# Optimization experiments

Hardware: AMD Instinct MI355X
Metric: run time of the kernel (lower is better)

The kernel has to match this reference:

```python
import jax, jax.numpy as jnp
import numpy as np

B, S, D, H, L, F = 4, 2048, 512, 8, 4, 2048
DH = D // H
EPS = 1e-5


def setup_inputs() -> dict:
    key = jax.random.key(0)
    ks = jax.random.split(key, 16)
    sc = 0.02
    inp = {
        "turn_embeddings": jax.random.normal(ks[0], (B, S, D), jnp.float32),
        "Wqkv": jax.random.normal(ks[1], (L, 3 * D, D), jnp.float32) * sc,
        "bqkv": jnp.zeros((L, 3 * D), jnp.float32),
        "Wo": jax.random.normal(ks[2], (L, D, D), jnp.float32) * sc,
        "bo": jnp.zeros((L, D), jnp.float32),
        "W1": jax.random.normal(ks[3], (L, F, D), jnp.float32) * sc,
        "b1": jnp.zeros((L, F), jnp.float32),
        "W2": jax.random.normal(ks[4], (L, D, F), jnp.float32) * sc,
        "b2": jnp.zeros((L, D), jnp.float32),
        "ln1_g": jnp.ones((L, D), jnp.float32),
        "ln1_b": jnp.zeros((L, D), jnp.float32),
        "ln2_g": jnp.ones((L, D), jnp.float32),
        "ln2_b": jnp.zeros((L, D), jnp.float32),
        "speaker_ids": jax.random.randint(ks[5], (B, S), 0, 4, jnp.int64 if jax.config.jax_enable_x64 else jnp.int32),
    }
    return inp


def _layer_norm(x, g, b):
    mu = jnp.mean(x, axis=-1, keepdims=True)
    var = jnp.mean(jnp.square(x - mu), axis=-1, keepdims=True)
    return (x - mu) * jax.lax.rsqrt(var + EPS) * g + b


def _attention(x, Wqkv, bqkv, Wo, bo, allow):
    # x: [B,S,D]; allow: [B,1,S,S] boolean (causal & same-speaker)
    qkv = x @ Wqkv.T + bqkv                       # [B,S,3D]
    q, k, v = jnp.split(qkv, 3, axis=-1)
    q = q.reshape(x.shape[0], x.shape[1], H, DH)
    k = k.reshape(x.shape[0], x.shape[1], H, DH)
    v = v.reshape(x.shape[0], x.shape[1], H, DH)
    scores = jnp.einsum("bqhd,bkhd->bhqk", q, k) / np.sqrt(DH)
    scores = jnp.where(allow, scores, jnp.finfo(scores.dtype).min)
    p = jax.nn.softmax(scores, axis=-1)
    o = jnp.einsum("bhqk,bkhd->bqhd", p, v).reshape(x.shape[0], x.shape[1], D)
    return o @ Wo.T + bo


def reference(turn_embeddings, Wqkv, bqkv, Wo, bo, W1, b1, W2, b2,
              ln1_g, ln1_b, ln2_g, ln2_b, speaker_ids):
    Bc, Sc, _ = turn_embeddings.shape
    causal = jnp.tril(jnp.ones((Sc, Sc), bool))                 # [S,S]
    same = speaker_ids[:, :, None] == speaker_ids[:, None, :]    # [B,S,S]
    allow = (same & causal)[:, None, :, :]                       # [B,1,S,S]
    x = turn_embeddings
    for l in range(L):
        a = _attention(x, Wqkv[l], bqkv[l], Wo[l], bo[l], allow)
        x = _layer_norm(x + a, ln1_g[l], ln1_b[l])
        h = jax.nn.relu(x @ W1[l].T + b1[l]) @ W2[l].T + b2[l]
        x = _layer_norm(x + h, ln2_g[l], ln2_b[l])
    return x
```

## Files before the change

### kernel.cpp

```cpp
#include <hip/hip_runtime.h>
#include <stdint.h>

#define BN 4
#define SN 2048
#define DN 512
#define HN 8
#define LN 4
#define FN 2048
#define MN (BN * SN)
#define TD (3 * DN)

typedef __attribute__((ext_vector_type(8))) __bf16 bf16x8;
typedef __attribute__((ext_vector_type(4))) float f32x4;
typedef __attribute__((ext_vector_type(8))) unsigned short ushortx8;

static __device__ __forceinline__ unsigned short f2bf(float f) {
    return __builtin_bit_cast(unsigned short, (__bf16)f);
}
static __device__ __forceinline__ float bf2f(unsigned short h) {
    return __builtin_bit_cast(float, (uint32_t)h << 16);
}

static __device__ __forceinline__ void gload16(const void* g, void* l) {
    __builtin_amdgcn_global_load_lds(
        (const __attribute__((address_space(1))) void*)g,
        (__attribute__((address_space(3))) void*)l, 16, 0, 0);
}

__global__ __launch_bounds__(256) void k_cvt_all(const float* __restrict__ Wqkv,
                                                 const float* __restrict__ Wo,
                                                 const float* __restrict__ W1,
                                                 const float* __restrict__ W2,
                                                 const float* __restrict__ te,
                                                 unsigned short* __restrict__ wqkv_b,
                                                 unsigned short* __restrict__ wo_b,
                                                 unsigned short* __restrict__ w1_b,
                                                 unsigned short* __restrict__ w2_b,
                                                 unsigned short* __restrict__ xb) {
    constexpr int G0 = LN * TD * DN / 4;
    constexpr int G1 = G0 + LN * DN * DN / 4;
    constexpr int G2 = G1 + LN * FN * DN / 4;
    constexpr int G3 = G2 + LN * DN * FN / 4;
    constexpr int G4 = G3 + MN * DN / 4;
    int i = blockIdx.x * blockDim.x + threadIdx.x;
    int stride = gridDim.x * blockDim.x;
    for (; i < G4; i += stride) {
        const float* s; unsigned short* d; int j;
        if (i < G0)      { s = Wqkv; d = wqkv_b; j = i; }
        else if (i < G1) { s = Wo;   d = wo_b;   j = i - G0; }
        else if (i < G2) { s = W1;   d = w1_b;   j = i - G1; }
        else if (i < G3) { s = W2;   d = w2_b;   j = i - G2; }
        else             { s = te;   d = xb;     j = i - G3; }
        float4 v = ((const float4*)s)[j];
        ushort4 o;
        o.x = f2bf(v.x); o.y = f2bf(v.y); o.z = f2bf(v.z); o.w = f2bf(v.w);
        ((ushort4*)d)[j] = o;
    }
}

template <int MODE, int BNT>
__global__ __launch_bounds__(256) void k_gemm(const unsigned short* __restrict__ A,
                                              const unsigned short* __restrict__ B,
                                              const float* __restrict__ bias,
                                              unsigned short* __restrict__ Cb,
                                              int M, int N, int K, int GX) {
    __shared__ __align__(16) unsigned short As[128][64];
    __shared__ __align__(16) unsigned short Bs[BNT][64];
    constexpr int NFR = BNT / 32;

    const int t = threadIdx.x;
    const int lane = t & 63;
    const int wid = t >> 6;
    const int wm = wid >> 1, wn = wid & 1;
    const int lr = lane & 15;
    const int lg = lane >> 4;

    const int nwg = gridDim.x;
    const int bid = blockIdx.x;
    const int swz = (bid & 7) * (nwg >> 3) + (bid >> 3);
    const int bx = swz % GX;
    const int by = swz / GX;

    const size_t rowA = (size_t)by * 128;
    const size_t rowB = (size_t)bx * BNT;
    const unsigned short* Ab = A + rowA * K;
    const unsigned short* Bb = B + rowB * K;

    const int srow = lane >> 3;
    const int sgran = (lane & 7) ^ srow;

    f32x4 acc[4][NFR] = {};

    for (int k0 = 0; k0 < K; k0 += 64) {
        __syncthreads();
#pragma unroll
        for (int j = 0; j < 4; ++j) {
            const int c = wid * 4 + j;
            const size_t goff = (size_t)(8 * c + srow) * K + k0 + sgran * 8;
            gload16(Ab + goff, &As[8 * c][0]);
        }
#pragma unroll
        for (int j = 0; j < NFR; ++j) {
            const int c = wid * NFR + j;
            const size_t goff = (size_t)(8 * c + srow) * K + k0 + sgran * 8;
            gload16(Bb + goff, &Bs[8 * c][0]);
        }
        __syncthreads();

#pragma unroll
        for (int h = 0; h < 2; ++h) {
            const int gp = (h * 4 + lg) ^ (lr & 7);
            bf16x8 af[4], bfr[NFR];
#pragma unroll
            for (int mi = 0; mi < 4; ++mi)
                af[mi] = *(const bf16x8*)&As[wm * 64 + mi * 16 + lr][gp * 8];
#pragma unroll
            for (int ni = 0; ni < NFR; ++ni)
                bfr[ni] = *(const bf16x8*)&Bs[wn * (BNT / 2) + ni * 16 + lr][gp * 8];
#pragma unroll
            for (int mi = 0; mi < 4; ++mi)
#pragma unroll
                for (int ni = 0; ni < NFR; ++ni)
                    acc[mi][ni] = __builtin_amdgcn_mfma_f32_16x16x32_bf16(
                        af[mi], bfr[ni], acc[mi][ni], 0, 0, 0);
        }
    }

    float bv[NFR];
#pragma unroll
    for (int ni = 0; ni < NFR; ++ni)
        bv[ni] = bias[(int)rowB + wn * (BNT / 2) + ni * 16 + lr];

#pragma unroll
    for (int mi = 0; mi < 4; ++mi) {
#pragma unroll
        for (int ni = 0; ni < NFR; ++ni) {
            int col = (int)rowB + wn * (BNT / 2) + ni * 16 + lr;
            int row0 = (int)rowA + wm * 64 + mi * 16 + lg * 4;
#pragma unroll
            for (int r = 0; r < 4; ++r) {
                float v = acc[mi][ni][r] + bv[ni];
                if (MODE == 2) v = fmaxf(v, 0.f);
                Cb[(size_t)(row0 + r) * N + col] = f2bf(v);
            }
        }
    }
}

__global__ __launch_bounds__(256) void k_attn(const unsigned short* __restrict__ qkv,
                                              const int* __restrict__ spk,
                                              unsigned short* __restrict__ o) {
    __shared__ __align__(16) unsigned short Ks[2][64][64];
    __shared__ __align__(16) unsigned short Vt[2][64][64];
    __shared__ __align__(16) unsigned short Ps[4][16][64];

    const int t = threadIdx.x;
    const int lane = t & 63;
    const int w = t >> 6;
    const int lr = lane & 15;
    const int lg = lane >> 4;
    const int l7 = lr & 7;

    const int wg = blockIdx.x;
    const int inner = wg >> 3;
    const int bh = 4 * (wg & 7) + (inner & 3);
    const int qtile = (SN / 64 - 1) - (inner >> 2);
    const int b = bh >> 3;
    const int h = bh & 7;
    const int qb = qtile * 64;

    const size_t base = (size_t)b * SN * TD;
    const unsigned short* kg = qkv + base + DN + h * 64;
    const unsigned short* vg = qkv + base + 2 * DN + h * 64;

    const float SCL = 0.125f * 1.4426950408889634f;
    const unsigned short* qptr = qkv + base + (size_t)(qb + w * 16 + lr) * TD + h * 64;
    bf16x8 aq0 = *(const bf16x8*)(qptr + lg * 8);
    bf16x8 aq1 = *(const bf16x8*)(qptr + 32 + lg * 8);
#pragma unroll
    for (int j = 0; j < 8; ++j) {
        aq0[j] = (__bf16)((float)aq0[j] * SCL);
        aq1[j] = (__bf16)((float)aq1[j] * SCL);
    }

    int sqr[4], qrow[4];
#pragma unroll
    for (int r = 0; r < 4; ++r) {
        qrow[r] = qb + w * 16 + lg * 4 + r;
        sqr[r] = spk[b * SN + qrow[r]];
    }

    const int krl = lane >> 3;
    const int kgran = (lane & 7) ^ krl;
    const int vrow = lane;
    const int vd0 = w * 16;

#pragma unroll
    for (int j = 0; j < 2; ++j)
        gload16(kg + (size_t)(w * 16 + j * 8 + krl) * TD + kgran * 8,
                &Ks[0][w * 16 + j * 8][0]);
    ushortx8 vra = *(const ushortx8*)&vg[(size_t)vrow * TD + vd0];
    ushortx8 vrb = *(const ushortx8*)&vg[(size_t)vrow * TD + vd0 + 8];
#pragma unroll
    for (int j = 0; j < 8; ++j) {
        const int vc0 = (((vrow >> 3) ^ j) << 3) + (vrow & 7);
        Vt[0][vd0 + j][vc0] = vra[j];
        Vt[0][vd0 + 8 + j][vc0] = vrb[j];
    }

    float lsum[4] = {0.f, 0.f, 0.f, 0.f};
    f32x4 acc_o[4] = {};

    const int ntiles = qtile + 1;
    for (int it = 0; it < ntiles; ++it) {
        const int k0 = it * 64;
        const int cur = it & 1;
        __syncthreads();

        const bool nx = (it + 1 < ntiles);
        if (nx) {
            const int kn = k0 + 64;
#pragma unroll
            for (int j = 0; j < 2; ++j)
                gload16(kg + (size_t)(kn + w * 16 + j * 8 + krl) * TD + kgran * 8,
                        &Ks[cur ^ 1][w * 16 + j * 8][0]);
            vra = *(const ushortx8*)&vg[(size_t)(kn + vrow) * TD + vd0];
            vrb = *(const ushortx8*)&vg[(size_t)(kn + vrow) * TD + vd0 + 8];
        }
        int skr[4];
#pragma unroll
        for (int ni = 0; ni < 4; ++ni) skr[ni] = spk[b * SN + k0 + 16 * ni + lr];

        f32x4 sc4[4] = {};
        __builtin_amdgcn_s_setprio(1);
#pragma unroll
        for (int ni = 0; ni < 4; ++ni) {
            bf16x8 bk0 = *(const bf16x8*)&Ks[cur][16 * ni + lr][(lg ^ l7) * 8];
            bf16x8 bk1 = *(const bf16x8*)&Ks[cur][16 * ni + lr][((lg + 4) ^ l7) * 8];
            sc4[ni] = __builtin_amdgcn_mfma_f32_16x16x32_bf16(aq0, bk0, sc4[ni], 0, 0, 0);
            sc4[ni] = __builtin_amdgcn_mfma_f32_16x16x32_bf16(aq1, bk1, sc4[ni], 0, 0, 0);
        }
        __builtin_amdgcn_s_setprio(0);

        const bool diag = (it == ntiles - 1);
#pragma unroll
        for (int ni = 0; ni < 4; ++ni) {
#pragma unroll
            for (int r = 0; r < 4; ++r) {
                bool allow = (skr[ni] == sqr[r]);
                if (diag) allow = allow && (16 * ni + lr <= w * 16 + lg * 4 + r);
                float p = allow ? __builtin_amdgcn_exp2f(sc4[ni][r]) : 0.f;
                lsum[r] += p;
                const int q7 = (lg * 4 + r) & 7;
                const int pg = ((2 * ni + (lr >> 3)) ^ q7) * 8 + l7;
                Ps[w][lg * 4 + r][pg] = f2bf(p);
            }
        }

        bf16x8 ap0 = *(const bf16x8*)&Ps[w][lr][(lg ^ l7) * 8];
        bf16x8 ap1 = *(const bf16x8*)&Ps[w][lr][((lg + 4) ^ l7) * 8];
        __builtin_amdgcn_s_setprio(1);
#pragma unroll
        for (int ni = 0; ni < 4; ++ni) {
            bf16x8 bv0 = *(const bf16x8*)&Vt[cur][16 * ni + lr][(lg ^ l7) * 8];
            bf16x8 bv1 = *(const bf16x8*)&Vt[cur][16 * ni + lr][((lg + 4) ^ l7) * 8];
            acc_o[ni] = __builtin_amdgcn_mfma_f32_16x16x32_bf16(ap0, bv0, acc_o[ni], 0, 0, 0);
            acc_o[ni] = __builtin_amdgcn_mfma_f32_16x16x32_bf16(ap1, bv1, acc_o[ni], 0, 0, 0);
        }
        __builtin_amdgcn_s_setprio(0);

        if (nx) {
            const int nb = cur ^ 1;
#pragma unroll
            for (int j = 0; j < 8; ++j) {
                const int vc0 = (((vrow >> 3) ^ j) << 3) + (vrow & 7);
                Vt[nb][vd0 + j][vc0] = vra[j];
                Vt[nb][vd0 + 8 + j][vc0] = vrb[j];
            }
        }
    }

#pragma unroll
    for (int r = 0; r < 4; ++r) {
        float s = lsum[r];
        s += __shfl_xor(s, 1);
        s += __shfl_xor(s, 2);
        s += __shfl_xor(s, 4);
        s += __shfl_xor(s, 8);
        float inv = 1.f / s;
#pragma unroll
        for (int ni = 0; ni < 4; ++ni) {
            int d = 16 * ni + lr;
            o[(size_t)(b * SN + qrow[r]) * DN + h * 64 + d] = f2bf(acc_o[ni][r] * inv);
        }
    }
}

template <bool XF32>
__global__ __launch_bounds__(256) void k_add_ln(const void* __restrict__ xin_,
                                                const unsigned short* __restrict__ dl,
                                                const float* __restrict__ g,
                                                const float* __restrict__ bta,
                                                unsigned short* __restrict__ xb,
                                                float* __restrict__ fout) {
    const int row = blockIdx.x * 4 + (threadIdx.x >> 6);
    const int lane = threadIdx.x & 63;
    const size_t off = (size_t)row * DN + lane * 8;
    const int c0 = lane * 8;

    float v[8];
    if (XF32) {
        const float* xin = (const float*)xin_;
        float4 a0 = *(const float4*)&xin[off];
        float4 a1 = *(const float4*)&xin[off + 4];
        v[0] = a0.x; v[1] = a0.y; v[2] = a0.z; v[3] = a0.w;
        v[4] = a1.x; v[5] = a1.y; v[6] = a1.z; v[7] = a1.w;
    } else {
        ushortx8 xa = *(const ushortx8*)&((const unsigned short*)xin_)[off];
#pragma unroll
        for (int i = 0; i < 8; ++i) v[i] = bf2f(xa[i]);
    }
    ushortx8 dd = *(const ushortx8*)&dl[off];
#pragma unroll
    for (int i = 0; i < 8; ++i) v[i] += bf2f(dd[i]);

    float s1 = 0.f, s2 = 0.f;
#pragma unroll
    for (int i = 0; i < 8; ++i) { s1 += v[i]; s2 += v[i] * v[i]; }
#pragma unroll
    for (int msk = 32; msk; msk >>= 1) {
        s1 += __shfl_xor(s1, msk);
        s2 += __shfl_xor(s2, msk);
    }
    const float mean = s1 * (1.f / 512.f);
    const float var = s2 * (1.f / 512.f) - mean * mean;
    const float rs = rsqrtf(var + 1e-5f);

    float4 g0 = *(const float4*)&g[c0];
    float4 g1 = *(const float4*)&g[c0 + 4];
    float4 b0 = *(const float4*)&bta[c0];
    float4 b1 = *(const float4*)&bta[c0 + 4];
    float gg[8] = {g0.x, g0.y, g0.z, g0.w, g1.x, g1.y, g1.z, g1.w};
    float bb[8] = {b0.x, b0.y, b0.z, b0.w, b1.x, b1.y, b1.z, b1.w};

    float y[8];
    ushortx8 ub;
#pragma unroll
    for (int i = 0; i < 8; ++i) {
        y[i] = (v[i] - mean) * rs * gg[i] + bb[i];
        ub[i] = f2bf(y[i]);
    }
    *(ushortx8*)&xb[off] = ub;
    if (fout) {
        *(float4*)&fout[off] = make_float4(y[0], y[1], y[2], y[3]);
        *(float4*)&fout[off + 4] = make_float4(y[4], y[5], y[6], y[7]);
    }
}

extern "C" void kernel_launch(void* const* d_in, const int* in_sizes, int n_in,
                              void* d_out, int out_size, void* d_ws, size_t ws_size,
                              hipStream_t stream) {
    const float* te   = (const float*)d_in[0];
    const float* Wqkv = (const float*)d_in[1];
    const float* bqkv = (const float*)d_in[2];
    const float* Wo   = (const float*)d_in[3];
    const float* bo   = (const float*)d_in[4];
    const float* W1   = (const float*)d_in[5];
    const float* b1   = (const float*)d_in[6];
    const float* W2   = (const float*)d_in[7];
    const float* b2   = (const float*)d_in[8];
    const float* g1   = (const float*)d_in[9];
    const float* be1  = (const float*)d_in[10];
    const float* g2   = (const float*)d_in[11];
    const float* be2  = (const float*)d_in[12];
    const int*   spk  = (const int*)d_in[13];
    float* out = (float*)d_out;

    char* ws = (char*)d_ws;
    size_t off = 0;
    auto alloc = [&](size_t bytes) -> char* {
        char* p = ws + off;
        off += (bytes + 255) & ~(size_t)255;
        return p;
    };
    unsigned short* wqkv_b = (unsigned short*)alloc((size_t)LN * TD * DN * 2);
    unsigned short* wo_b   = (unsigned short*)alloc((size_t)LN * DN * DN * 2);
    unsigned short* w1_b   = (unsigned short*)alloc((size_t)LN * FN * DN * 2);
    unsigned short* w2_b   = (unsigned short*)alloc((size_t)LN * DN * FN * 2);
    unsigned short* xb     = (unsigned short*)alloc((size_t)MN * DN * 2);
    unsigned short* u      = (unsigned short*)alloc((size_t)MN * FN * 2);
    unsigned short* ob     = (unsigned short*)alloc((size_t)MN * DN * 2);
    unsigned short* projb  = (unsigned short*)alloc((size_t)MN * DN * 2);
    unsigned short* qkvb = u;
    unsigned short* hb   = u;

    k_cvt_all<<<2048, 256, 0, stream>>>(Wqkv, Wo, W1, W2, te,
                                        wqkv_b, wo_b, w1_b, w2_b, xb);

    for (int l = 0; l < LN; ++l) {
        k_gemm<1, 128><<<(MN / 128) * (TD / 128), 256, 0, stream>>>(
            xb, wqkv_b + (size_t)l * TD * DN, bqkv + l * TD, qkvb,
            MN, TD, DN, TD / 128);
        k_attn<<<(SN / 64) * BN * HN, 256, 0, stream>>>(qkvb, spk, ob);
        k_gemm<1, 64><<<(MN / 128) * (DN / 64), 256, 0, stream>>>(
            ob, wo_b + (size_t)l * DN * DN, bo + l * DN, projb,
            MN, DN, DN, DN / 64);
        if (l == 0)
            k_add_ln<true><<<MN / 4, 256, 0, stream>>>(
                te, projb, g1 + l * DN, be1 + l * DN, xb, nullptr);
        else
            k_add_ln<false><<<MN / 4, 256, 0, stream>>>(
                xb, projb, g1 + l * DN, be1 + l * DN, xb, nullptr);
        k_gemm<2, 128><<<(MN / 128) * (FN / 128), 256, 0, stream>>>(
            xb, w1_b + (size_t)l * FN * DN, b1 + l * FN, hb,
            MN, FN, DN, FN / 128);
        k_gemm<1, 64><<<(MN / 128) * (DN / 64), 256, 0, stream>>>(
            hb, w2_b + (size_t)l * DN * FN, b2 + l * DN, projb,
            MN, DN, FN, DN / 64);
        k_add_ln<false><<<MN / 4, 256, 0, stream>>>(
            xb, projb, g2 + l * DN, be2 + l * DN, xb,
            (l == LN - 1) ? out : nullptr);
    }
    (void)in_sizes; (void)n_in; (void)out_size; (void)ws_size;
}
```

Before: 606.6 us.

## Transpose QK^T MFMA so each lane owns one query row in attention

Swaps the MFMA operand order so the score tile comes out transposed: each lane holds four consecutive keys for a single query row. The speaker-id check, causal mask and row-sum then work on one query per lane, so the per-row cross-lane reduction becomes two shuffles and P is written to LDS as packed 8-byte stores instead of scalar 2-byte ones. K tiles are now loaded through registers and written to LDS after the PV step, replacing the direct global-to-LDS loads. The register round-trip costs extra VGPRs and LDS write instructions in exchange for fewer LDS stores and shuffles.

```diff
diff --git a/kernel.cpp b/kernel.cpp
--- a/kernel.cpp
+++ b/kernel.cpp
@@ -172,9 +172,11 @@
     const size_t base = (size_t)b * SN * TD;
     const unsigned short* kg = qkv + base + DN + h * 64;
     const unsigned short* vg = qkv + base + 2 * DN + h * 64;
+    const int* spb = spk + b * SN;
 
     const float SCL = 0.125f * 1.4426950408889634f;
-    const unsigned short* qptr = qkv + base + (size_t)(qb + w * 16 + lr) * TD + h * 64;
+    const int qrow_t = qb + w * 16 + lr;
+    const unsigned short* qptr = qkv + base + (size_t)qrow_t * TD + h * 64;
     bf16x8 aq0 = *(const bf16x8*)(qptr + lg * 8);
     bf16x8 aq1 = *(const bf16x8*)(qptr + 32 + lg * 8);
 #pragma unroll
@@ -182,25 +184,19 @@
         aq0[j] = (__bf16)((float)aq0[j] * SCL);
         aq1[j] = (__bf16)((float)aq1[j] * SCL);
     }
-
-    int sqr[4], qrow[4];
-#pragma unroll
-    for (int r = 0; r < 4; ++r) {
-        qrow[r] = qb + w * 16 + lg * 4 + r;
-        sqr[r] = spk[b * SN + qrow[r]];
-    }
-
-    const int krl = lane >> 3;
-    const int kgran = (lane & 7) ^ krl;
+    const int sq = spb[qrow_t];
+
+    const int kr0 = t >> 3;
+    const int kgr = ((t & 7) ^ (kr0 & 7)) * 8;
     const int vrow = lane;
     const int vd0 = w * 16;
 
-#pragma unroll
-    for (int j = 0; j < 2; ++j)
-        gload16(kg + (size_t)(w * 16 + j * 8 + krl) * TD + kgran * 8,
-                &Ks[0][w * 16 + j * 8][0]);
+    uint4 kra = *(const uint4*)&kg[(size_t)kr0 * TD + (t & 7) * 8];
+    uint4 krb = *(const uint4*)&kg[(size_t)(kr0 + 32) * TD + (t & 7) * 8];
     ushortx8 vra = *(const ushortx8*)&vg[(size_t)vrow * TD + vd0];
     ushortx8 vrb = *(const ushortx8*)&vg[(size_t)vrow * TD + vd0 + 8];
+    *(uint4*)&Ks[0][kr0][kgr] = kra;
+    *(uint4*)&Ks[0][kr0 + 32][kgr] = krb;
 #pragma unroll
     for (int j = 0; j < 8; ++j) {
         const int vc0 = (((vrow >> 3) ^ j) << 3) + (vrow & 7);
@@ -208,7 +204,7 @@
         Vt[0][vd0 + 8 + j][vc0] = vrb[j];
     }
 
-    float lsum[4] = {0.f, 0.f, 0.f, 0.f};
+    float lsum = 0.f;
     f32x4 acc_o[4] = {};
 
     const int ntiles = qtile + 1;
@@ -220,41 +216,45 @@
         const bool nx = (it + 1 < ntiles);
         if (nx) {
             const int kn = k0 + 64;
-#pragma unroll
-            for (int j = 0; j < 2; ++j)
-                gload16(kg + (size_t)(kn + w * 16 + j * 8 + krl) * TD + kgran * 8,
-                        &Ks[cur ^ 1][w * 16 + j * 8][0]);
+            kra = *(const uint4*)&kg[(size_t)(kn + kr0) * TD + (t & 7) * 8];
+            krb = *(const uint4*)&kg[(size_t)(kn + kr0 + 32) * TD + (t & 7) * 8];
             vra = *(const ushortx8*)&vg[(size_t)(kn + vrow) * TD + vd0];
             vrb = *(const ushortx8*)&vg[(size_t)(kn + vrow) * TD + vd0 + 8];
         }
-        int skr[4];
-#pragma unroll
-        for (int ni = 0; ni < 4; ++ni) skr[ni] = spk[b * SN + k0 + 16 * ni + lr];
+        int4 kk[4];
+#pragma unroll
+        for (int ni = 0; ni < 4; ++ni)
+            kk[ni] = *(const int4*)&spb[k0 + 16 * ni + lg * 4];
 
         f32x4 sc4[4] = {};
         __builtin_amdgcn_s_setprio(1);
 #pragma unroll
         for (int ni = 0; ni < 4; ++ni) {
-            bf16x8 bk0 = *(const bf16x8*)&Ks[cur][16 * ni + lr][(lg ^ l7) * 8];
-            bf16x8 bk1 = *(const bf16x8*)&Ks[cur][16 * ni + lr][((lg + 4) ^ l7) * 8];
-            sc4[ni] = __builtin_amdgcn_mfma_f32_16x16x32_bf16(aq0, bk0, sc4[ni], 0, 0, 0);
-            sc4[ni] = __builtin_amdgcn_mfma_f32_16x16x32_bf16(aq1, bk1, sc4[ni], 0, 0, 0);
+            bf16x8 ak0 = *(const bf16x8*)&Ks[cur][16 * ni + lr][(lg ^ l7) * 8];
+            bf16x8 ak1 = *(const bf16x8*)&Ks[cur][16 * ni + lr][((lg + 4) ^ l7) * 8];
+            sc4[ni] = __builtin_amdgcn_mfma_f32_16x16x32_bf16(ak0, aq0, sc4[ni], 0, 0, 0);
+            sc4[ni] = __builtin_amdgcn_mfma_f32_16x16x32_bf16(ak1, aq1, sc4[ni], 0, 0, 0);
         }
         __builtin_amdgcn_s_setprio(0);
 
         const bool diag = (it == ntiles - 1);
 #pragma unroll
         for (int ni = 0; ni < 4; ++ni) {
+            const int kb = 16 * ni + lg * 4;
+            int sk[4] = {kk[ni].x, kk[ni].y, kk[ni].z, kk[ni].w};
+            float p[4];
 #pragma unroll
             for (int r = 0; r < 4; ++r) {
-                bool allow = (skr[ni] == sqr[r]);
-                if (diag) allow = allow && (16 * ni + lr <= w * 16 + lg * 4 + r);
-                float p = allow ? __builtin_amdgcn_exp2f(sc4[ni][r]) : 0.f;
-                lsum[r] += p;
-                const int q7 = (lg * 4 + r) & 7;
-                const int pg = ((2 * ni + (lr >> 3)) ^ q7) * 8 + l7;
-                Ps[w][lg * 4 + r][pg] = f2bf(p);
+                bool allow = (sk[r] == sq);
+                if (diag) allow = allow && (kb + r <= w * 16 + lr);
+                p[r] = allow ? __builtin_amdgcn_exp2f(sc4[ni][r]) : 0.f;
+                lsum += p[r];
             }
+            uint32_t u0 = (uint32_t)f2bf(p[0]) | ((uint32_t)f2bf(p[1]) << 16);
+            uint32_t u1 = (uint32_t)f2bf(p[2]) | ((uint32_t)f2bf(p[3]) << 16);
+            const int G = (2 * ni + (lg >> 1)) ^ l7;
+            uint2 pu; pu.x = u0; pu.y = u1;
+            *(uint2*)&Ps[w][lr][G * 8 + (lg & 1) * 4] = pu;
         }
 
         bf16x8 ap0 = *(const bf16x8*)&Ps[w][lr][(lg ^ l7) * 8];
@@ -271,6 +271,8 @@
 
         if (nx) {
             const int nb = cur ^ 1;
+            *(uint4*)&Ks[nb][kr0][kgr] = kra;
+            *(uint4*)&Ks[nb][kr0 + 32][kgr] = krb;
 #pragma unroll
             for (int j = 0; j < 8; ++j) {
                 const int vc0 = (((vrow >> 3) ^ j) << 3) + (vrow & 7);
@@ -280,18 +282,18 @@
         }
     }
 
+    lsum += __shfl_xor(lsum, 16);
+    lsum += __shfl_xor(lsum, 32);
+    const float inv = 1.f / lsum;
+
 #pragma unroll
     for (int r = 0; r < 4; ++r) {
-        float s = lsum[r];
-        s += __shfl_xor(s, 1);
-        s += __shfl_xor(s, 2);
-        s += __shfl_xor(s, 4);
-        s += __shfl_xor(s, 8);
-        float inv = 1.f / s;
+        const float invr = __shfl(inv, lg * 4 + r);
+        const int q = qb + w * 16 + lg * 4 + r;
 #pragma unroll
         for (int ni = 0; ni < 4; ++ni) {
             int d = 16 * ni + lr;
-            o[(size_t)(b * SN + qrow[r]) * DN + h * 64 + d] = f2bf(acc_o[ni][r] * inv);
+            o[(size_t)(b * SN + q) * DN + h * 64 + d] = f2bf(acc_o[ni][r] * invr);
         }
     }
 }
```

Result: no change. 611.8 us (+0.9%).

## Double-buffer GEMM LDS tiles with BK=32 and register-stage K loads in attention

Applied to the files above, without the earlier changes.

The GEMM kernel changes from a single-buffered BK=64 loop with two barriers per step to a double-buffered BK=32 pipeline, so the global-to-LDS loads for the next K slice run during the MFMAs on the current one. LDS footprint stays about the same, but the loop now takes twice as many iterations and has a narrower XOR swizzle. In the attention kernel, K tiles are now read through registers with ordinary global loads and written to LDS after the PV step, like V, instead of using async global_load_lds. This is meant to let K loads overlap compute and remove the LDS-DMA hazard wait, at the cost of extra registers and explicit LDS stores.

```diff
diff --git a/kernel.cpp b/kernel.cpp
--- a/kernel.cpp
+++ b/kernel.cpp
@@ -64,9 +64,10 @@
                                               const float* __restrict__ bias,
                                               unsigned short* __restrict__ Cb,
                                               int M, int N, int K, int GX) {
-    __shared__ __align__(16) unsigned short As[128][64];
-    __shared__ __align__(16) unsigned short Bs[BNT][64];
+    __shared__ __align__(16) unsigned short As[2][128][32];
+    __shared__ __align__(16) unsigned short Bs[2][BNT][32];
     constexpr int NFR = BNT / 32;
+    constexpr int BCH = BNT / 16;
 
     const int t = threadIdx.x;
     const int lane = t & 63;
@@ -74,6 +75,7 @@
     const int wm = wid >> 1, wn = wid & 1;
     const int lr = lane & 15;
     const int lg = lane >> 4;
+    const int l3 = lr & 3;
 
     const int nwg = gridDim.x;
     const int bid = blockIdx.x;
@@ -86,44 +88,59 @@
     const unsigned short* Ab = A + rowA * K;
     const unsigned short* Bb = B + rowB * K;
 
-    const int srow = lane >> 3;
-    const int sgran = (lane & 7) ^ srow;
+    const int srow = lane >> 2;
+    const int sgran = (lane & 3) ^ (srow & 3);
 
     f32x4 acc[4][NFR] = {};
 
-    for (int k0 = 0; k0 < K; k0 += 64) {
+    const int nit = K >> 5;
+
+#pragma unroll
+    for (int j = 0; j < 2; ++j) {
+        const int c = wid * 2 + j;
+        gload16(Ab + (size_t)(16 * c + srow) * K + sgran * 8, &As[0][16 * c][0]);
+    }
+#pragma unroll
+    for (int j = 0; j < BCH / 4; ++j) {
+        const int c = wid * (BCH / 4) + j;
+        gload16(Bb + (size_t)(16 * c + srow) * K + sgran * 8, &Bs[0][16 * c][0]);
+    }
+    __syncthreads();
+
+    for (int it = 0; it < nit; ++it) {
+        const int cur = it & 1;
+        if (it + 1 < nit) {
+            const int k0 = (it + 1) << 5;
+#pragma unroll
+            for (int j = 0; j < 2; ++j) {
+                const int c = wid * 2 + j;
+                gload16(Ab + (size_t)(16 * c + srow) * K + k0 + sgran * 8,
+                        &As[cur ^ 1][16 * c][0]);
+            }
+#pragma unroll
+            for (int j = 0; j < BCH / 4; ++j) {
+                const int c = wid * (BCH / 4) + j;
+                gload16(Bb + (size_t)(16 * c + srow) * K + k0 + sgran * 8,
+                        &Bs[cur ^ 1][16 * c][0]);
+            }
+        }
+
+        const int gp = (lg ^ l3) * 8;
+        bf16x8 af[4], bfr[NFR];
+#pragma unroll
+        for (int mi = 0; mi < 4; ++mi)
+            af[mi] = *(const bf16x8*)&As[cur][wm * 64 + mi * 16 + lr][gp];
+#pragma unroll
+        for (int ni = 0; ni < NFR; ++ni)
+            bfr[ni] = *(const bf16x8*)&Bs[cur][wn * (BNT / 2) + ni * 16 + lr][gp];
+#pragma unroll
+        for (int mi = 0; mi < 4; ++mi)
+#pragma unroll
+            for (int ni = 0; ni < NFR; ++ni)
+                acc[mi][ni] = __builtin_amdgcn_mfma_f32_16x16x32_bf16(
+                    af[mi], bfr[ni], acc[mi][ni], 0, 0, 0);
+
         __syncthreads();
-#pragma unroll
-        for (int j = 0; j < 4; ++j) {
-            const int c = wid * 4 + j;
-            const size_t goff = (size_t)(8 * c + srow) * K + k0 + sgran * 8;
-            gload16(Ab + goff, &As[8 * c][0]);
-        }
-#pragma unroll
-        for (int j = 0; j < NFR; ++j) {
-            const int c = wid * NFR + j;
-            const size_t goff = (size_t)(8 * c + srow) * K + k0 + sgran * 8;
-            gload16(Bb + goff, &Bs[8 * c][0]);
-        }
-        __syncthreads();
-
-#pragma unroll
-        for (int h = 0; h < 2; ++h) {
-            const int gp = (h * 4 + lg) ^ (lr & 7);
-            bf16x8 af[4], bfr[NFR];
-#pragma unroll
-            for (int mi = 0; mi < 4; ++mi)
-                af[mi] = *(const bf16x8*)&As[wm * 64 + mi * 16 + lr][gp * 8];
-#pragma unroll
-            for (int ni = 0; ni < NFR; ++ni)
-                bfr[ni] = *(const bf16x8*)&Bs[wn * (BNT / 2) + ni * 16 + lr][gp * 8];
-#pragma unroll
-            for (int mi = 0; mi < 4; ++mi)
-#pragma unroll
-                for (int ni = 0; ni < NFR; ++ni)
-                    acc[mi][ni] = __builtin_amdgcn_mfma_f32_16x16x32_bf16(
-                        af[mi], bfr[ni], acc[mi][ni], 0, 0, 0);
-        }
     }
 
     float bv[NFR];
@@ -190,17 +207,17 @@
         sqr[r] = spk[b * SN + qrow[r]];
     }
 
-    const int krl = lane >> 3;
-    const int kgran = (lane & 7) ^ krl;
-    const int vrow = lane;
-    const int vd0 = w * 16;
-
-#pragma unroll
-    for (int j = 0; j < 2; ++j)
-        gload16(kg + (size_t)(w * 16 + j * 8 + krl) * TD + kgran * 8,
-                &Ks[0][w * 16 + j * 8][0]);
+    const int kr0 = t >> 3;
+    const int kgr = ((t & 7) ^ (kr0 & 7)) * 8;
+    const int vrow = t & 63;
+    const int vd0 = (t >> 6) * 16;
+
+    uint4 kra = *(const uint4*)&kg[(size_t)kr0 * TD + (t & 7) * 8];
+    uint4 krb = *(const uint4*)&kg[(size_t)(kr0 + 32) * TD + (t & 7) * 8];
     ushortx8 vra = *(const ushortx8*)&vg[(size_t)vrow * TD + vd0];
     ushortx8 vrb = *(const ushortx8*)&vg[(size_t)vrow * TD + vd0 + 8];
+    *(uint4*)&Ks[0][kr0][kgr] = kra;
+    *(uint4*)&Ks[0][kr0 + 32][kgr] = krb;
 #pragma unroll
     for (int j = 0; j < 8; ++j) {
         const int vc0 = (((vrow >> 3) ^ j) << 3) + (vrow & 7);
@@ -220,10 +237,8 @@
         const bool nx = (it + 1 < ntiles);
         if (nx) {
             const int kn = k0 + 64;
-#pragma unroll
-            for (int j = 0; j < 2; ++j)
-                gload16(kg + (size_t)(kn + w * 16 + j * 8 + krl) * TD + kgran * 8,
-                        &Ks[cur ^ 1][w * 16 + j * 8][0]);
+            kra = *(const uint4*)&kg[(size_t)(kn + kr0) * TD + (t & 7) * 8];
+            krb = *(const uint4*)&kg[(size_t)(kn + kr0 + 32) * TD + (t & 7) * 8];
             vra = *(const ushortx8*)&vg[(size_t)(kn + vrow) * TD + vd0];
             vrb = *(const ushortx8*)&vg[(size_t)(kn + vrow) * TD + vd0 + 8];
         }
@@ -271,6 +286,8 @@
 
         if (nx) {
             const int nb = cur ^ 1;
+            *(uint4*)&Ks[nb][kr0][kgr] = kra;
+            *(uint4*)&Ks[nb][kr0 + 32][kgr] = krb;
 #pragma unroll
             for (int j = 0; j < 8; ++j) {
                 const int vc0 = (((vrow >> 3) ^ j) << 3) + (vrow & 7);
```

After: 637.2 us. +5.0%, slower.
